# Kernel tuning notes

Measured on AMD Instinct MI355X. Metric: run time of the kernel, lower is better.

The kernel has to match this reference:

```python
import jax, jax.numpy as jnp
import numpy as np

KS = 7
ITERS = 6
B, C, H, W = 2, 64, 256, 1216

_WM7 = [1,1,1,1,1,1,1,1,0,0,0,0,0,1,1,0,0,0,0,0,1,1,0,0,0,0,0,1,1,0,0,0,0,0,1,1,0,0,0,0,0,1,1,1,1,1,1,1,1]
_WM5 = [0,0,0,0,0,0,0,0,1,1,1,1,1,0,0,1,0,0,0,1,0,0,1,0,0,0,1,0,0,1,0,0,0,1,0,0,1,1,1,1,1,0,0,0,0,0,0,0,0]
_WM3 = [0,0,0,0,0,0,0,0,0,0,0,0,0,0,0,0,1,1,1,0,0,0,0,1,0,1,0,0,0,0,1,1,1,0,0,0,0,0,0,0,0,0,0,0,0,0,0,0,0]

# per 7x7 position t: which guide tensor (ring) and which channel within it
_SRC = []
_i7 = _i5 = _i3 = 0
for _t in range(KS * KS):
    if _WM7[_t]:
        _SRC.append(("7", _i7)); _i7 += 1
    elif _WM5[_t]:
        _SRC.append(("5", _i5)); _i5 += 1
    elif _WM3[_t]:
        _SRC.append(("3", _i3)); _i3 += 1
    else:
        _SRC.append(("1", 0))


def _convbn(x, w, s, b):
    # Conv2d(bias=False) + BatchNorm2d (inference) folded to per-channel scale/bias.
    y = jax.lax.conv_general_dilated(x, w, window_strides=(1, 1),
                                     padding=((1, 1), (1, 1)),
                                     dimension_numbers=("NCHW", "OIHW", "NCHW"))
    return y * s[None, :, None, None] + b[None, :, None, None]


def setup_inputs() -> dict:
    key = jax.random.key(0)
    ks = iter(jax.random.split(key, 64))
    def nrm(shape, scale=1.0):
        return jax.random.normal(next(ks), shape, jnp.float32) * scale
    def uni(shape):
        return jax.random.uniform(next(ks), shape, dtype=jnp.float32)
    inp = {
        "feature": nrm((B, C, H, W)),
        "d0": uni((B, 1, H, W)),
        "d00": nrm((B, 1, H, W)),  # ~half positive -> mixed valid_mask
    }
    layers = [("aff7", 24), ("aff5", 16), ("aff3", 8),
              ("att7", 6), ("att5", 6), ("att3", 6), ("att1", 6), ("mask", 6)]
    fan = 1.0 / np.sqrt(C * 9)
    for name, out in layers:
        inp["w_" + name] = nrm((out, C, 3, 3), fan)
        inp["s_" + name] = uni((out,))
        inp["b_" + name] = nrm((out,), 0.1)
    return inp


def reference(feature, d0, d00,
              w_aff7, s_aff7, b_aff7, w_aff5, s_aff5, b_aff5, w_aff3, s_aff3, b_aff3,
              w_att7, s_att7, b_att7, w_att5, s_att5, b_att5, w_att3, s_att3, b_att3,
              w_att1, s_att1, b_att1, w_mask, s_mask, b_mask):
    valid = (d00 > 0).astype(d00.dtype)
    mask_all = jax.nn.sigmoid(_convbn(feature, w_mask, s_mask, b_mask)) * valid
    aff7 = _convbn(feature, w_aff7, s_aff7, b_aff7)  # [B,24,H,W]
    aff5 = _convbn(feature, w_aff5, s_aff5, b_aff5)  # [B,16,H,W]
    aff3 = _convbn(feature, w_aff3, s_aff3, b_aff3)  # [B, 8,H,W]
    att7 = jax.nn.sigmoid(_convbn(feature, w_att7, s_att7, b_att7))
    att5 = jax.nn.sigmoid(_convbn(feature, w_att5, s_att5, b_att5))
    att3 = jax.nn.sigmoid(_convbn(feature, w_att3, s_att3, b_att3))
    att1 = jax.nn.sigmoid(_convbn(feature, w_att1, s_att1, b_att1))

    dt = d0
    for it in range(ITERS):
        mask = mask_all[:, it:it + 1]
        g7 = att7[:, it:it + 1] * aff7
        g5 = att5[:, it:it + 1] * aff5
        g3 = att3[:, it:it + 1] * aff3
        g1 = att1[:, it:it + 1]
        denom = (jnp.sum(jnp.abs(g7), 1, keepdims=True)
                 + jnp.sum(jnp.abs(g5), 1, keepdims=True)
                 + jnp.sum(jnp.abs(g3), 1, keepdims=True)
                 + jnp.abs(g1))
        g7, g5, g3, g1 = g7 / denom, g5 / denom, g3 / denom, g1 / denom
        g0 = 1.0 - (jnp.sum(g7, 1, keepdims=True) + jnp.sum(g5, 1, keepdims=True)
                    + jnp.sum(g3, 1, keepdims=True) + g1)
        guides = {"7": g7, "5": g5, "3": g3, "1": g1}
        # scatter ring guides into full 49-channel 7x7 layout
        G = jnp.concatenate([guides[k][:, i:i + 1] for k, i in _SRC], axis=1)  # [B,49,H,W]
        # weighted neighbor gather: out(p) = sum_t G_t(p+off_t) * dt(p+off_t)
        P = G * dt  # [B,49,H,W]
        Pp = jnp.pad(P, ((0, 0), (0, 0), (3, 3), (3, 3)))
        acc = jnp.zeros_like(dt)
        for t in range(KS * KS):
            i, j = t // KS, t % KS
            acc = acc + Pp[:, t:t + 1, 6 - i:6 - i + H, 6 - j:6 - j + W]
        dt = acc + g0 * d0
        dt = mask * d00 + (1.0 - mask) * dt
    return dt
```

## Files before the change

kernel.cpp:

```cpp
#include <hip/hip_runtime.h>
#include <hip/hip_fp16.h>
#include <stdint.h>

#define HH 256
#define WW 1216
#define BB 2
#define CC 64
#define IPIX (HH*WW)
#define NPIX (BB*IPIX)
#define PW 1280
#define PH 262
#define PPIX (PH*PW)
#define PLSTRIDE (BB*PPIX)
#define XOFF 32

typedef __attribute__((ext_vector_type(8))) __bf16 bf16x8;
typedef __attribute__((ext_vector_type(4))) __bf16 bf16x4;
typedef __attribute__((ext_vector_type(4))) float floatx4;
typedef __attribute__((ext_vector_type(4))) _Float16 half4;

__device__ __forceinline__ float sigm(float x) { return 1.f / (1.f + __expf(-x)); }

constexpr int LSTART_H[9] = {0,24,40,48,54,60,66,72,78};

constexpr int PLANE[49] = {
  0, 1, 2, 3, 4, 5, 6,
  7,24,25,26,27,28, 8,
  9,29,40,41,42,30,10,
 11,31,43,-1,44,32,12,
 13,33,45,46,47,34,14,
 15,35,36,37,38,39,16,
 17,18,19,20,21,22,23};
constexpr int KCLS[49] = {
 0,0,0,0,0,0,0,
 0,1,1,1,1,1,0,
 0,1,2,2,2,1,0,
 0,1,2,3,2,1,0,
 0,1,2,2,2,1,0,
 0,1,1,1,1,1,0,
 0,0,0,0,0,0,0};
constexpr int TAPNC[48] = {
  0,1,2,3,4,5,6,7,8,9,10,11,12,13,14,15,16,17,18,19,20,21,22,23,
  25,26,27,28,29,30,31,32,33,34,35,36,37,38,39,40,41,42,43,44,45,46,47,48};

struct WPtrs {
    const float* w[8];
    const float* s[8];
    const float* b[8];
};

__global__ void k_pack(WPtrs wp, __bf16* __restrict__ wpk,
                       float* __restrict__ s_all, float* __restrict__ b_all) {
    int idx = blockIdx.x * blockDim.x + threadIdx.x;
    if (idx < 18 * 5 * 64) {
        int kk = idx / (5 * 64);
        int r = idx - kk * 5 * 64;
        int t = r >> 6, lane = r & 63;
        int m = t * 16 + (lane & 15);
        int L = 0, o = 0;
        bool valid_m = (m < 78);
        if (valid_m) {
            for (int i = 0; i < 8; i++) if (m >= LSTART_H[i]) { L = i; o = m - LSTART_H[i]; }
        }
        __bf16 vals[8];
        for (int j = 0; j < 8; j++) {
            int k = kk * 32 + ((lane >> 4) * 8) + j;
            int tap = k >> 6, c = k & 63;
            float w = valid_m ? wp.w[L][(o * 64 + c) * 9 + tap] : 0.f;
            vals[j] = (__bf16)w;
        }
        for (int j = 0; j < 8; j++) wpk[(size_t)idx * 8 + j] = vals[j];
    }
    if (idx < 80) {
        int m = idx;
        float sv = 0.f, bv = 0.f;
        if (m < 78) {
            int L = 0, o = 0;
            for (int i = 0; i < 8; i++) if (m >= LSTART_H[i]) { L = i; o = m - LSTART_H[i]; }
            sv = wp.s[L][o]; bv = wp.b[L][o];
        }
        s_all[m] = sv; b_all[m] = bv;
    }
}

__global__ void k_zero_pad(__bf16* __restrict__ aff_p) {
    const int perPB = 6 * PW + 256 * 16;
    int idx = blockIdx.x * blockDim.x + threadIdx.x;
    int total = 48 * BB * perPB;
    if (idx >= total) return;
    int pbi = idx / perPB;
    int e = idx - pbi * perPB;
    int plane = pbi >> 1, b = pbi & 1;
    int r, c;
    if (e < 6 * PW) {
        int rr = e / PW; c = e - rr * PW;
        r = (rr < 3) ? rr : (259 + rr - 3);
    } else {
        int j = e - 6 * PW;
        r = 3 + (j >> 4);
        int c16 = j & 15;
        c = (c16 < 8) ? (24 + c16) : (1248 + c16 - 8);
    }
    aff_p[(size_t)plane * PLSTRIDE + (size_t)b * PPIX + r * PW + c] = (__bf16)0.f;
}

__global__ __launch_bounds__(256) void k_cvt(const float* __restrict__ feat,
                                             __bf16* __restrict__ fpk) {
    const int x = blockIdx.x * 64 + (threadIdx.x & 63);
    const int half = threadIdx.x >> 6;
    const int y = blockIdx.y, b = blockIdx.z;
    const float* fb = feat + (size_t)b * CC * IPIX + (size_t)y * WW + x;
    __bf16* op = fpk + ((size_t)(b * IPIX + y * WW + x) << 6);
#pragma unroll
    for (int h = 0; h < 2; h++) {
        const int cg = half + h * 4;
        bf16x8 pk;
#pragma unroll
        for (int j = 0; j < 8; j++) pk[j] = (__bf16)fb[(size_t)(cg * 8 + j) * IPIX];
        *(bf16x8*)(op + cg * 8) = pk;
    }
}

__global__ __launch_bounds__(256, 4) void k_conv(const __bf16* __restrict__ fpk,
        const float* __restrict__ d00, const __bf16* __restrict__ wpk,
        const float* __restrict__ s_all, const float* __restrict__ b_all,
        __bf16* __restrict__ aff_p, __bf16* __restrict__ attp, __bf16* __restrict__ maskp,
        float* __restrict__ stp) {
    __shared__ __bf16 sh[6 * 34 * 72];
    __shared__ __bf16 wlds[2 * 2560];
    const int tid = threadIdx.x;
    int flat = blockIdx.x + 38 * (blockIdx.y + 64 * blockIdx.z);
    int nf = (flat & 7) * 608 + (flat >> 3);
    int bx = nf % 38; int r2 = nf / 38;
    const int x0 = bx * 32, y0 = (r2 & 63) * 4, b = r2 >> 6;

    {
        bf16x8 w0 = *(const bf16x8*)(wpk + (size_t)tid * 8);
        *(bf16x8*)(wlds + tid * 8) = w0;
        if (tid < 64) {
            bf16x8 w1 = *(const bf16x8*)(wpk + 2048 + (size_t)tid * 8);
            *(bf16x8*)(wlds + 2048 + tid * 8) = w1;
        }
    }
    for (int idx = tid; idx < 204 * 8; idx += 256) {
        int cg = idx & 7, pos = idx >> 3;
        int row = pos / 34, x = pos - row * 34;
        int gy = y0 + row - 1, gx = x0 + x - 1;
        bf16x8 pk;
#pragma unroll
        for (int j = 0; j < 8; j++) pk[j] = (__bf16)0.f;
        if (gy >= 0 && gy < HH && gx >= 0 && gx < WW)
            pk = *(const bf16x8*)(fpk + ((size_t)(b * IPIX + gy * WW + gx) << 6) + cg * 8);
        *(bf16x8*)(sh + pos * 72 + cg * 8) = pk;
    }
    __syncthreads();

    const int wave = tid >> 6, lane = tid & 63;
    const int n = lane & 15, g = lane >> 4;

    floatx4 acc[5][2];
#pragma unroll
    for (int t = 0; t < 5; t++)
#pragma unroll
        for (int q = 0; q < 2; q++) acc[t][q] = (floatx4)(0.f);

#pragma unroll
    for (int kk = 0; kk < 18; kk++) {
        bf16x8 wt0, wt1;
        if (kk < 17) {
            wt0 = *(const bf16x8*)(wpk + (size_t)(kk + 1) * 2560 + tid * 8);
            if (tid < 64) wt1 = *(const bf16x8*)(wpk + (size_t)(kk + 1) * 2560 + 2048 + tid * 8);
        }
        const int tap = kk >> 1;
        const int dy = tap / 3 - 1, dx = tap % 3 - 1;
        const int c0 = (kk & 1) * 32 + g * 8;
        bf16x8 bfr[2];
        const int rowb = wave + 1 + dy;
        const int colb = 1 + dx + n;
#pragma unroll
        for (int q = 0; q < 2; q++)
            bfr[q] = *(const bf16x8*)(sh + ((rowb * 34) + colb + q * 16) * 72 + c0);
        bf16x8 afr[5];
        const __bf16* wb = wlds + (kk & 1) * 2560 + lane * 8;
#pragma unroll
        for (int t = 0; t < 5; t++) afr[t] = *(const bf16x8*)(wb + t * 512);
#pragma unroll
        for (int t = 0; t < 5; t++)
#pragma unroll
            for (int q = 0; q < 2; q++)
                acc[t][q] = __builtin_amdgcn_mfma_f32_16x16x32_bf16(afr[t], bfr[q], acc[t][q], 0, 0, 0);
        if (kk < 17) {
            *(bf16x8*)(wlds + ((kk + 1) & 1) * 2560 + tid * 8) = wt0;
            if (tid < 64) *(bf16x8*)(wlds + ((kk + 1) & 1) * 2560 + 2048 + tid * 8) = wt1;
        }
        __syncthreads();
    }

    const int pix_base = b * IPIX + (y0 + wave) * WW + x0 + n;
    float p7[2] = {0,0}, t7[2] = {0,0};
    float p5[2] = {0,0}, t5[2] = {0,0};
    float p3[2] = {0,0}, t3[2] = {0,0};

#pragma unroll
    for (int t = 0; t < 5; t++) {
        const floatx4 sv = *(const floatx4*)(s_all + t * 16 + 4 * g);
        const floatx4 bv = *(const floatx4*)(b_all + t * 16 + 4 * g);
#pragma unroll
        for (int q = 0; q < 2; q++) {
#pragma unroll
            for (int reg = 0; reg < 4; reg++) {
                const int m = t * 16 + 4 * g + reg;
                const float v = fmaf(acc[t][q][reg], sv[reg], bv[reg]);
                if (m < 24)                { p7[q] += fabsf(v); t7[q] += v; }
                else if (m < 40)           { p5[q] += fabsf(v); t5[q] += v; }
                else if (m < 48)           { p3[q] += fabsf(v); t3[q] += v; }
                const float outv = (m < 48) ? v : sigm(v);
                sh[m * 132 + wave * 32 + n + q * 16] = (__bf16)outv;
            }
        }
    }
#pragma unroll
    for (int q = 0; q < 2; q++) {
        p7[q] += __shfl_xor(p7[q], 16); p7[q] += __shfl_xor(p7[q], 32);
        t7[q] += __shfl_xor(t7[q], 16); t7[q] += __shfl_xor(t7[q], 32);
        p5[q] += __shfl_xor(p5[q], 16); p5[q] += __shfl_xor(p5[q], 32);
        t5[q] += __shfl_xor(t5[q], 16); t5[q] += __shfl_xor(t5[q], 32);
        p3[q] += __shfl_xor(p3[q], 16); p3[q] += __shfl_xor(p3[q], 32);
        t3[q] += __shfl_xor(t3[q], 16); t3[q] += __shfl_xor(t3[q], 32);
    }
    if (g == 0) {
#pragma unroll
        for (int q = 0; q < 2; q++) {
            const int pixq = pix_base + q * 16;
            floatx4 s0 = {p7[q], p5[q], p3[q], t7[q]};
            floatx4 s1 = {t5[q], t3[q], 0.f, 0.f};
            *(floatx4*)(stp + (size_t)pixq * 8)     = s0;
            *(floatx4*)(stp + (size_t)pixq * 8 + 4) = s1;
        }
    }
    __syncthreads();

    const int px = tid & 127;
    const int grp = tid >> 7;
    const int prow = px >> 5, pcol = px & 31;
    const size_t ppx = (size_t)b * PPIX + (y0 + prow + 3) * PW + (x0 + pcol + XOFF);
    const int pix = b * IPIX + (y0 + prow) * WW + x0 + pcol;
#pragma unroll
    for (int m = 0; m < 48; m += 2) {
        aff_p[(size_t)(m + grp) * PLSTRIDE + ppx] = sh[(m + grp) * 132 + px];
    }
    const float d00v = d00[pix];
    const float valid = (d00v > 0.f) ? 1.f : 0.f;
#pragma unroll
    for (int j = 0; j < 6; j += 2) {
        const int it = j + grp;
        bf16x4 av = { sh[(48 + it) * 132 + px], sh[(54 + it) * 132 + px],
                      sh[(60 + it) * 132 + px], sh[(66 + it) * 132 + px] };
        *(bf16x4*)(attp + ((size_t)it * NPIX + pix) * 4) = av;
        maskp[(size_t)it * NPIX + pix] = (__bf16)((float)sh[(72 + it) * 132 + px] * valid);
    }
}

__global__ __launch_bounds__(256) void k_rg(const __bf16* __restrict__ attp,
        const float* __restrict__ stp, const float* __restrict__ d0,
        _Float16* __restrict__ rp, float* __restrict__ gd) {
    int g = blockIdx.x * blockDim.x + threadIdx.x;
    if (g >= NPIX) return;
    const floatx4 s0 = *(const floatx4*)(stp + (size_t)g * 8);
    const floatx4 s1 = *(const floatx4*)(stp + (size_t)g * 8 + 4);
    const float S7 = s0[0], S5 = s0[1], S3 = s0[2], T7 = s0[3], T5 = s1[0], T3 = s1[1];
    const float d0v = d0[g];
#pragma unroll
    for (int it = 0; it < 6; it++) {
        bf16x4 a = *(const bf16x4*)(attp + ((size_t)it * NPIX + g) * 4);
        float a7 = (float)a[0], a5 = (float)a[1], a3 = (float)a[2], a1 = (float)a[3];
        float denom = a7 * S7 + a5 * S5 + a3 * S3 + a1;
        float inv = 1.f / denom;
        float r7 = a7 * inv, r5 = a5 * inv, r3 = a3 * inv, r1 = a1 * inv;
        float g0 = 1.f - (r7 * T7 + r5 * T5 + r3 * T3 + r1);
        half4 rv = {(_Float16)r7, (_Float16)r5, (_Float16)r3, (_Float16)r1};
        *(half4*)(rp + ((size_t)it * NPIX + g) * 4) = rv;
        gd[(size_t)it * NPIX + g] = g0 * d0v;
    }
}

__global__ __launch_bounds__(256) void k_iter(const _Float16* __restrict__ rp,
        const float* __restrict__ gd, const float* __restrict__ dt,
        const __bf16* __restrict__ aff_p, const __bf16* __restrict__ maskp,
        const float* __restrict__ d00,
        float* __restrict__ dtn, int it) {
    __shared__ float sp[5][14 * 38];
    const int tid = threadIdx.x;
    const int tx = tid & 31, ty = tid >> 5;
    int flat = blockIdx.x + 38 * (blockIdx.y + 32 * blockIdx.z);
    int nf = (flat & 7) * 304 + (flat >> 3);
    int bx = nf % 38; int r2 = nf / 38;
    const int x0 = bx * 32, y0 = (r2 & 31) * 8, b = r2 >> 5;
    const int ib = b * IPIX;

    for (int idx = tid; idx < 14 * 38; idx += 256) {
        int r = idx / 38, col = idx - r * 38;
        int gy = y0 + r - 3, gx = x0 + col - 3;
        float v7 = 0.f, v5 = 0.f, v3 = 0.f, v1 = 0.f, vb = 0.f;
        if (gy >= 0 && gy < HH && gx >= 0 && gx < WW) {
            int q = ib + gy * WW + gx;
            half4 rv = *(const half4*)(rp + ((size_t)it * NPIX + q) * 4);
            float dtv = dt[q];
            v7 = (float)rv[0] * dtv; v5 = (float)rv[1] * dtv;
            v3 = (float)rv[2] * dtv; v1 = (float)rv[3] * dtv;
            vb = gd[(size_t)it * NPIX + q];
        }
        sp[0][idx] = v7; sp[1][idx] = v5; sp[2][idx] = v3; sp[3][idx] = v1; sp[4][idx] = vb;
    }
    __syncthreads();

    const int y = y0 + ty, x = x0 + tx;
    const int pix = ib + y * WW + x;
    const __bf16* ap = aff_p + (size_t)b * PPIX + (y + 3) * PW + (x + XOFF);

    float acc0 = sp[4][(ty + 3) * 38 + (tx + 3)] + sp[3][(ty + 3) * 38 + (tx + 3)];
    float acc1 = 0.f, acc2 = 0.f, acc3 = 0.f;
#pragma unroll
    for (int bt = 0; bt < 6; bt++) {
        float a8[8];
#pragma unroll
        for (int j = 0; j < 8; j++) {
            const int t = TAPNC[bt * 8 + j];
            const int dy = 3 - t / 7, dx = 3 - (t % 7);
            a8[j] = (float)ap[(ptrdiff_t)PLANE[t] * PLSTRIDE + dy * PW + dx];
        }
#pragma unroll
        for (int j = 0; j < 8; j++) {
            const int t = TAPNC[bt * 8 + j];
            const int dy = 3 - t / 7, dx = 3 - (t % 7);
            const float pv = sp[KCLS[t]][(ty + dy + 3) * 38 + (tx + dx + 3)];
            switch (j & 3) {
                case 0: acc0 = fmaf(a8[j], pv, acc0); break;
                case 1: acc1 = fmaf(a8[j], pv, acc1); break;
                case 2: acc2 = fmaf(a8[j], pv, acc2); break;
                default: acc3 = fmaf(a8[j], pv, acc3); break;
            }
        }
    }
    float acc = (acc0 + acc1) + (acc2 + acc3);
    float m = (float)maskp[(size_t)it * NPIX + pix];
    float dtv = m * d00[pix] + (1.f - m) * acc;
    dtn[pix] = dtv;
}

extern "C" void kernel_launch(void* const* d_in, const int* in_sizes, int n_in,
                              void* d_out, int out_size, void* d_ws, size_t ws_size,
                              hipStream_t stream) {
    const float* feat = (const float*)d_in[0];
    const float* d0   = (const float*)d_in[1];
    const float* d00  = (const float*)d_in[2];
    WPtrs wp;
    for (int l = 0; l < 8; l++) {
        wp.w[l] = (const float*)d_in[3 + 3 * l];
        wp.s[l] = (const float*)d_in[4 + 3 * l];
        wp.b[l] = (const float*)d_in[5 + 3 * l];
    }
    __bf16*   wsb   = (__bf16*)d_ws;
    __bf16*   aff_p = wsb;
    __bf16*   attp  = aff_p + (size_t)48 * PLSTRIDE;
    __bf16*   msk_b = attp + (size_t)24 * NPIX;
    float*    stp   = (float*)(msk_b + (size_t)6 * NPIX);
    float*    dtA   = stp + (size_t)8 * NPIX;
    __bf16*   wpk   = (__bf16*)(dtA + (size_t)NPIX);
    float*    s_all = (float*)(wpk + 18 * 5 * 64 * 8);
    float*    b_all = s_all + 80;
    char*     X     = (char*)(b_all + 80);
    __bf16*   fpk   = (__bf16*)X;
    _Float16* rp    = (_Float16*)X;
    float*    gd    = (float*)(X + (size_t)24 * NPIX * 2);
    float*    dtB   = (float*)d_out;

    hipLaunchKernelGGL(k_pack, dim3(23), dim3(256), 0, stream, wp, wpk, s_all, b_all);
    hipLaunchKernelGGL(k_zero_pad, dim3((48 * BB * (6 * PW + 256 * 16) + 255) / 256), dim3(256),
                       0, stream, aff_p);
    hipLaunchKernelGGL(k_cvt, dim3(WW / 64, HH, BB), dim3(256), 0, stream, feat, fpk);
    hipLaunchKernelGGL(k_conv, dim3(38, 64, 2), dim3(256), 0, stream,
                       fpk, d00, wpk, s_all, b_all, aff_p, attp, msk_b, stp);
    hipLaunchKernelGGL(k_rg, dim3(NPIX / 256), dim3(256), 0, stream,
                       attp, stp, d0, rp, gd);
    const float* cur = d0;
    for (int it = 0; it < 6; ++it) {
        float* nxt = (it & 1) ? dtB : dtA;
        if (it == 5) nxt = dtB;
        hipLaunchKernelGGL(k_iter, dim3(38, 32, 2), dim3(256), 0, stream,
                           rp, gd, cur, aff_p, msk_b, d00, nxt, it);
        cur = nxt;
    }
}
```

Baseline: 522.5 us.

## Fuse guide normalization into conv epilogue and enlarge iteration tiles

Moves the per-pixel normalization (denominator, ratios, g0*d0) from the separate k_rg kernel into the k_conv epilogue. Row sums now pass through shared memory instead of global staging, and the intermediate att and stats buffers are gone. The ratios and gd term are packed into one 16-byte record per pixel per iteration, so k_iter does a single vector load. k_iter tiles grow from 8 to 16 rows with 512 threads, which cuts the halo overhead. This costs more LDS use and register pressure in k_conv, and the 16-byte record carries 4 bytes of padding.

```diff
diff --git a/kernel.cpp b/kernel.cpp
--- a/kernel.cpp
+++ b/kernel.cpp
@@ -17,7 +17,6 @@
 typedef __attribute__((ext_vector_type(8))) __bf16 bf16x8;
 typedef __attribute__((ext_vector_type(4))) __bf16 bf16x4;
 typedef __attribute__((ext_vector_type(4))) float floatx4;
-typedef __attribute__((ext_vector_type(4))) _Float16 half4;
 
 __device__ __forceinline__ float sigm(float x) { return 1.f / (1.f + __expf(-x)); }
 
@@ -122,10 +121,11 @@
 }
 
 __global__ __launch_bounds__(256, 4) void k_conv(const __bf16* __restrict__ fpk,
-        const float* __restrict__ d00, const __bf16* __restrict__ wpk,
+        const float* __restrict__ d00, const float* __restrict__ d0,
+        const __bf16* __restrict__ wpk,
         const float* __restrict__ s_all, const float* __restrict__ b_all,
-        __bf16* __restrict__ aff_p, __bf16* __restrict__ attp, __bf16* __restrict__ maskp,
-        float* __restrict__ stp) {
+        __bf16* __restrict__ aff_p, __bf16* __restrict__ maskp,
+        float* __restrict__ rgd) {
     __shared__ __bf16 sh[6 * 34 * 72];
     __shared__ __bf16 wlds[2 * 2560];
     const int tid = threadIdx.x;
@@ -196,7 +196,6 @@
         __syncthreads();
     }
 
-    const int pix_base = b * IPIX + (y0 + wave) * WW + x0 + n;
     float p7[2] = {0,0}, t7[2] = {0,0};
     float p5[2] = {0,0}, t5[2] = {0,0};
     float p3[2] = {0,0}, t3[2] = {0,0};
@@ -228,14 +227,13 @@
         p3[q] += __shfl_xor(p3[q], 16); p3[q] += __shfl_xor(p3[q], 32);
         t3[q] += __shfl_xor(t3[q], 16); t3[q] += __shfl_xor(t3[q], 32);
     }
+    float* stl = (float*)(sh + 10560);
     if (g == 0) {
 #pragma unroll
         for (int q = 0; q < 2; q++) {
-            const int pixq = pix_base + q * 16;
-            floatx4 s0 = {p7[q], p5[q], p3[q], t7[q]};
-            floatx4 s1 = {t5[q], t3[q], 0.f, 0.f};
-            *(floatx4*)(stp + (size_t)pixq * 8)     = s0;
-            *(floatx4*)(stp + (size_t)pixq * 8 + 4) = s1;
+            const int pxq = wave * 32 + n + q * 16;
+            stl[pxq * 6 + 0] = p7[q]; stl[pxq * 6 + 1] = p5[q]; stl[pxq * 6 + 2] = p3[q];
+            stl[pxq * 6 + 3] = t7[q]; stl[pxq * 6 + 4] = t5[q]; stl[pxq * 6 + 5] = t3[q];
         }
     }
     __syncthreads();
@@ -249,66 +247,57 @@
     for (int m = 0; m < 48; m += 2) {
         aff_p[(size_t)(m + grp) * PLSTRIDE + ppx] = sh[(m + grp) * 132 + px];
     }
-    const float d00v = d00[pix];
-    const float valid = (d00v > 0.f) ? 1.f : 0.f;
+    const float S7 = stl[px * 6 + 0], S5 = stl[px * 6 + 1], S3 = stl[px * 6 + 2];
+    const float T7 = stl[px * 6 + 3], T5 = stl[px * 6 + 4], T3 = stl[px * 6 + 5];
+    const float d0v = d0[pix];
+    const float valid = (d00[pix] > 0.f) ? 1.f : 0.f;
 #pragma unroll
     for (int j = 0; j < 6; j += 2) {
         const int it = j + grp;
-        bf16x4 av = { sh[(48 + it) * 132 + px], sh[(54 + it) * 132 + px],
-                      sh[(60 + it) * 132 + px], sh[(66 + it) * 132 + px] };
-        *(bf16x4*)(attp + ((size_t)it * NPIX + pix) * 4) = av;
-        maskp[(size_t)it * NPIX + pix] = (__bf16)((float)sh[(72 + it) * 132 + px] * valid);
-    }
-}
-
-__global__ __launch_bounds__(256) void k_rg(const __bf16* __restrict__ attp,
-        const float* __restrict__ stp, const float* __restrict__ d0,
-        _Float16* __restrict__ rp, float* __restrict__ gd) {
-    int g = blockIdx.x * blockDim.x + threadIdx.x;
-    if (g >= NPIX) return;
-    const floatx4 s0 = *(const floatx4*)(stp + (size_t)g * 8);
-    const floatx4 s1 = *(const floatx4*)(stp + (size_t)g * 8 + 4);
-    const float S7 = s0[0], S5 = s0[1], S3 = s0[2], T7 = s0[3], T5 = s1[0], T3 = s1[1];
-    const float d0v = d0[g];
-#pragma unroll
-    for (int it = 0; it < 6; it++) {
-        bf16x4 a = *(const bf16x4*)(attp + ((size_t)it * NPIX + g) * 4);
-        float a7 = (float)a[0], a5 = (float)a[1], a3 = (float)a[2], a1 = (float)a[3];
+        float a7 = (float)sh[(48 + it) * 132 + px];
+        float a5 = (float)sh[(54 + it) * 132 + px];
+        float a3 = (float)sh[(60 + it) * 132 + px];
+        float a1 = (float)sh[(66 + it) * 132 + px];
         float denom = a7 * S7 + a5 * S5 + a3 * S3 + a1;
         float inv = 1.f / denom;
         float r7 = a7 * inv, r5 = a5 * inv, r3 = a3 * inv, r1 = a1 * inv;
         float g0 = 1.f - (r7 * T7 + r5 * T5 + r3 * T3 + r1);
-        half4 rv = {(_Float16)r7, (_Float16)r5, (_Float16)r3, (_Float16)r1};
-        *(half4*)(rp + ((size_t)it * NPIX + g) * 4) = rv;
-        gd[(size_t)it * NPIX + g] = g0 * d0v;
-    }
-}
-
-__global__ __launch_bounds__(256) void k_iter(const _Float16* __restrict__ rp,
-        const float* __restrict__ gd, const float* __restrict__ dt,
+        union { float f; _Float16 h[2]; } w0, w1;
+        w0.h[0] = (_Float16)r7; w0.h[1] = (_Float16)r5;
+        w1.h[0] = (_Float16)r3; w1.h[1] = (_Float16)r1;
+        floatx4 rec = {w0.f, w1.f, g0 * d0v, 0.f};
+        *(floatx4*)(rgd + ((size_t)it * NPIX + pix) * 4) = rec;
+        maskp[(size_t)it * NPIX + pix] = (__bf16)((float)sh[(72 + it) * 132 + px] * valid);
+    }
+}
+
+__global__ __launch_bounds__(512) void k_iter(const float* __restrict__ rgd,
+        const float* __restrict__ dt,
         const __bf16* __restrict__ aff_p, const __bf16* __restrict__ maskp,
         const float* __restrict__ d00,
         float* __restrict__ dtn, int it) {
-    __shared__ float sp[5][14 * 38];
+    __shared__ float sp[5][22 * 38];
     const int tid = threadIdx.x;
     const int tx = tid & 31, ty = tid >> 5;
-    int flat = blockIdx.x + 38 * (blockIdx.y + 32 * blockIdx.z);
-    int nf = (flat & 7) * 304 + (flat >> 3);
+    int flat = blockIdx.x + 38 * (blockIdx.y + 16 * blockIdx.z);
+    int nf = (flat & 7) * 152 + (flat >> 3);
     int bx = nf % 38; int r2 = nf / 38;
-    const int x0 = bx * 32, y0 = (r2 & 31) * 8, b = r2 >> 5;
+    const int x0 = bx * 32, y0 = (r2 & 15) * 16, b = r2 >> 4;
     const int ib = b * IPIX;
 
-    for (int idx = tid; idx < 14 * 38; idx += 256) {
+    for (int idx = tid; idx < 22 * 38; idx += 512) {
         int r = idx / 38, col = idx - r * 38;
         int gy = y0 + r - 3, gx = x0 + col - 3;
         float v7 = 0.f, v5 = 0.f, v3 = 0.f, v1 = 0.f, vb = 0.f;
         if (gy >= 0 && gy < HH && gx >= 0 && gx < WW) {
             int q = ib + gy * WW + gx;
-            half4 rv = *(const half4*)(rp + ((size_t)it * NPIX + q) * 4);
+            const floatx4 v = *(const floatx4*)(rgd + ((size_t)it * NPIX + q) * 4);
+            union { float f; _Float16 h[2]; } u0, u1;
+            u0.f = v[0]; u1.f = v[1];
             float dtv = dt[q];
-            v7 = (float)rv[0] * dtv; v5 = (float)rv[1] * dtv;
-            v3 = (float)rv[2] * dtv; v1 = (float)rv[3] * dtv;
-            vb = gd[(size_t)it * NPIX + q];
+            v7 = (float)u0.h[0] * dtv; v5 = (float)u0.h[1] * dtv;
+            v3 = (float)u1.h[0] * dtv; v1 = (float)u1.h[1] * dtv;
+            vb = v[2];
         }
         sp[0][idx] = v7; sp[1][idx] = v5; sp[2][idx] = v3; sp[3][idx] = v1; sp[4][idx] = vb;
     }
@@ -362,17 +351,13 @@
     }
     __bf16*   wsb   = (__bf16*)d_ws;
     __bf16*   aff_p = wsb;
-    __bf16*   attp  = aff_p + (size_t)48 * PLSTRIDE;
-    __bf16*   msk_b = attp + (size_t)24 * NPIX;
-    float*    stp   = (float*)(msk_b + (size_t)6 * NPIX);
-    float*    dtA   = stp + (size_t)8 * NPIX;
+    __bf16*   msk_b = aff_p + (size_t)48 * PLSTRIDE;
+    float*    rgd   = (float*)(msk_b + (size_t)6 * NPIX);
+    float*    dtA   = rgd + (size_t)24 * NPIX;
     __bf16*   wpk   = (__bf16*)(dtA + (size_t)NPIX);
     float*    s_all = (float*)(wpk + 18 * 5 * 64 * 8);
     float*    b_all = s_all + 80;
-    char*     X     = (char*)(b_all + 80);
-    __bf16*   fpk   = (__bf16*)X;
-    _Float16* rp    = (_Float16*)X;
-    float*    gd    = (float*)(X + (size_t)24 * NPIX * 2);
+    __bf16*   fpk   = (__bf16*)(b_all + 80);
     float*    dtB   = (float*)d_out;
 
     hipLaunchKernelGGL(k_pack, dim3(23), dim3(256), 0, stream, wp, wpk, s_all, b_all);
@@ -380,15 +365,13 @@
                        0, stream, aff_p);
     hipLaunchKernelGGL(k_cvt, dim3(WW / 64, HH, BB), dim3(256), 0, stream, feat, fpk);
     hipLaunchKernelGGL(k_conv, dim3(38, 64, 2), dim3(256), 0, stream,
-                       fpk, d00, wpk, s_all, b_all, aff_p, attp, msk_b, stp);
-    hipLaunchKernelGGL(k_rg, dim3(NPIX / 256), dim3(256), 0, stream,
-                       attp, stp, d0, rp, gd);
+                       fpk, d00, d0, wpk, s_all, b_all, aff_p, msk_b, rgd);
     const float* cur = d0;
     for (int it = 0; it < 6; ++it) {
         float* nxt = (it & 1) ? dtB : dtA;
         if (it == 5) nxt = dtB;
-        hipLaunchKernelGGL(k_iter, dim3(38, 32, 2), dim3(256), 0, stream,
-                           rp, gd, cur, aff_p, msk_b, d00, nxt, it);
+        hipLaunchKernelGGL(k_iter, dim3(38, 16, 2), dim3(512), 0, stream,
+                           rgd, cur, aff_p, msk_b, d00, nxt, it);
         cur = nxt;
     }
 }
```

Result: slower. 537.7 us (+2.9%).
